# Performance work log

Hardware: AMD Instinct MI355X
Metric: run time of the kernel (lower is better)

Reference implementation:

```python
import jax, jax.numpy as jnp
import numpy as np

D = 1024
H = 16
HD = D // H
B = 2
T = 2048


def _rope_tables(t, hd):
    inv_freq = 1.0 / (10000.0 ** (np.arange(0, hd, 2, dtype=np.float32) / hd))
    ang = np.arange(t, dtype=np.float32)[:, None] * inv_freq[None, :]  # [T, hd/2]
    emb = np.concatenate([ang, ang], axis=-1)  # [T, hd]
    return jnp.asarray(np.cos(emb)), jnp.asarray(np.sin(emb))


def setup_inputs() -> dict:
    key = jax.random.key(0)
    kx, kq, kk, kv, ko = jax.random.split(key, 5)
    scale = 0.02
    x = jax.random.normal(kx, (B, T, D), dtype=jnp.float32)
    cos, sin = _rope_tables(T, HD)
    mask = jnp.tril(jnp.ones((T, T), dtype=jnp.int32))[None, None]  # [1,1,T,T]
    wq = jax.random.normal(kq, (D, D), dtype=jnp.float32) * scale
    wk = jax.random.normal(kk, (D, D), dtype=jnp.float32) * scale
    wv = jax.random.normal(kv, (D, D), dtype=jnp.float32) * scale
    wo = jax.random.normal(ko, (D, D), dtype=jnp.float32) * scale
    return {"x": x, "cos": cos, "sin": sin, "mask": mask,
            "wq": wq, "wk": wk, "wv": wv, "wo": wo}


def _rotate_half(t):
    t1, t2 = jnp.split(t, 2, axis=-1)
    return jnp.concatenate((-t2, t1), axis=-1)


def reference(x, cos, sin, mask, wq, wk, wv, wo):
    Bx, Tx, C = x.shape
    hd = C // H
    # nn.Linear: y = x @ W.T  -> [B,T,H,hd] -> [B,H,T,hd]
    q = (x @ wq.T).reshape(Bx, Tx, H, hd).transpose(0, 2, 1, 3)
    k = (x @ wk.T).reshape(Bx, Tx, H, hd).transpose(0, 2, 1, 3)
    v = (x @ wv.T).reshape(Bx, Tx, H, hd).transpose(0, 2, 1, 3)
    c = cos[:Tx][None, None]  # [1,1,T,hd]
    s = sin[:Tx][None, None]
    q = q * c + _rotate_half(q) * s
    k = k * c + _rotate_half(k) * s
    att = jnp.einsum('bhqd,bhkd->bhqk', q, k) * (hd ** -0.5)
    att = jnp.where(mask[:, :, :Tx, :Tx] == 0, -jnp.inf, att)
    att = jax.nn.softmax(att, axis=-1)
    out = jnp.einsum('bhqk,bhkd->bhqd', att, v)
    out = out.transpose(0, 2, 1, 3).reshape(Bx, Tx, C)
    return out @ wo.T
```

## Files before the change

kernel.cpp:

```cpp
#include <hip/hip_runtime.h>
#include <math.h>

constexpr int D  = 1024;
constexpr int H  = 16;
constexpr int HD = 64;
constexpr int B  = 2;
constexpr int T  = 2048;
constexpr int M  = B * T;

constexpr size_t XSZ = (size_t)M * D;
constexpr size_t WSZ = (size_t)D * D;

typedef float  f32x4   __attribute__((ext_vector_type(4)));
typedef float  f32x16  __attribute__((ext_vector_type(16)));
typedef __bf16 bf16x8  __attribute__((ext_vector_type(8)));
typedef __bf16 bf16x4  __attribute__((ext_vector_type(4)));
typedef unsigned u32x2 __attribute__((ext_vector_type(2)));
typedef unsigned u32x4 __attribute__((ext_vector_type(4)));

static __device__ inline f32x4 mfma16(bf16x8 a, bf16x8 b, f32x4 c) {
  return __builtin_amdgcn_mfma_f32_16x16x32_bf16(a, b, c, 0, 0, 0);
}
static __device__ inline f32x16 mfma32(bf16x8 a, bf16x8 b, f32x16 c) {
  return __builtin_amdgcn_mfma_f32_32x32x16_bf16(a, b, c, 0, 0, 0);
}
static __device__ inline unsigned cvtpk(float a, float b) {
  unsigned r;
  asm("v_cvt_pk_bf16_f32 %0, %1, %2" : "=v"(r) : "v"(a), "v"(b));
  return r;
}
static __device__ inline u32x2 plswap(unsigned a, unsigned b) {
  return __builtin_amdgcn_permlane32_swap(a, b, false, false);
}
static __device__ inline void gload16(const __bf16* g, __bf16* l) {
  __builtin_amdgcn_global_load_lds(
      (const __attribute__((address_space(1))) void*)g,
      (__attribute__((address_space(3))) void*)l, 16, 0, 0);
}

__global__ __launch_bounds__(256)
void cvt_all(const float* __restrict__ x, const float* __restrict__ wq,
             const float* __restrict__ wk, const float* __restrict__ wv,
             const float* __restrict__ wo, __bf16* __restrict__ out) {
  size_t idx = ((size_t)blockIdx.x * 256 + threadIdx.x) * 8;
  const float* src;
  if      (idx < XSZ)            src = x  + idx;
  else if (idx < XSZ + WSZ)      src = wq + (idx - XSZ);
  else if (idx < XSZ + 2 * WSZ)  src = wk + (idx - XSZ - WSZ);
  else if (idx < XSZ + 3 * WSZ)  src = wv + (idx - XSZ - 2 * WSZ);
  else                           src = wo + (idx - XSZ - 3 * WSZ);
  float4 a = *reinterpret_cast<const float4*>(src);
  float4 b = *reinterpret_cast<const float4*>(src + 4);
  bf16x8 o;
  o[0] = (__bf16)a.x; o[1] = (__bf16)a.y; o[2] = (__bf16)a.z; o[3] = (__bf16)a.w;
  o[4] = (__bf16)b.x; o[5] = (__bf16)b.y; o[6] = (__bf16)b.z; o[7] = (__bf16)b.w;
  *reinterpret_cast<bf16x8*>(out + idx) = o;
}

template<int MODE>
__global__ __launch_bounds__(256)
void gemm_mfma(const __bf16* __restrict__ A,
               const __bf16* __restrict__ W0, const __bf16* __restrict__ W1,
               const __bf16* __restrict__ W2,
               const float* __restrict__ cosT, const float* __restrict__ sinT,
               void* __restrict__ out0, void* __restrict__ out1,
               void* __restrict__ out2) {
  __shared__ __bf16 As[128 * 64];
  __shared__ __bf16 Bs[128 * 64];

  const int tid  = threadIdx.x;
  const int lane = tid & 63;
  const int w    = tid >> 6;
  const int wm   = w >> 1;
  const int wn   = w & 1;
  const int l15  = lane & 15, lg = lane >> 4;
  const int m0   = blockIdx.y * 128;

  int which, n0;
  const __bf16* Bw;
  if (MODE == 1) {
    which = blockIdx.x >> 3;
    n0 = (blockIdx.x & 7) * 128;
    Bw = which == 0 ? W0 : which == 1 ? W1 : W2;
  } else {
    which = 0;
    n0 = blockIdx.x * 128;
    Bw = W0;
  }

  f32x4 acc[4][4];
  #pragma unroll
  for (int i = 0; i < 4; ++i)
    #pragma unroll
    for (int j = 0; j < 4; ++j) acc[i][j] = (f32x4){0.f, 0.f, 0.f, 0.f};

  const int r0 = tid >> 3;
  const int c0 = (tid & 7) * 8;

  for (int k0 = 0; k0 < 1024; k0 += 64) {
    #pragma unroll
    for (int i = 0; i < 4; ++i) {
      gload16(A  + (size_t)(m0 + r0 + 32 * i) * 1024 + k0 + c0,
              As + (tid + 256 * i) * 8);
      gload16(Bw + (size_t)(n0 + r0 + 32 * i) * 1024 + k0 + c0,
              Bs + (tid + 256 * i) * 8);
    }
    __syncthreads();

    #pragma unroll
    for (int ks = 0; ks < 2; ++ks) {
      bf16x8 af[4], bfr[4];
      #pragma unroll
      for (int mt = 0; mt < 4; ++mt)
        af[mt] = *reinterpret_cast<const bf16x8*>(
            &As[(wm * 64 + mt * 16 + l15) * 64 + ks * 32 + lg * 8]);
      #pragma unroll
      for (int nt = 0; nt < 4; ++nt)
        bfr[nt] = *reinterpret_cast<const bf16x8*>(
            &Bs[(wn * 64 + nt * 16 + l15) * 64 + ks * 32 + lg * 8]);
      #pragma unroll
      for (int mt = 0; mt < 4; ++mt)
        #pragma unroll
        for (int nt = 0; nt < 4; ++nt)
          acc[mt][nt] = mfma16(af[mt], bfr[nt], acc[mt][nt]);
    }
    __syncthreads();
  }

  if (MODE == 0) {
    float* o = (float*)out0;
    #pragma unroll
    for (int mt = 0; mt < 4; ++mt) {
      const int mb = m0 + wm * 64 + mt * 16 + lg * 4;
      #pragma unroll
      for (int nt = 0; nt < 4; ++nt) {
        const int n = n0 + wn * 64 + nt * 16 + l15;
        #pragma unroll
        for (int r = 0; r < 4; ++r)
          o[(size_t)(mb + r) * 1024 + n] = acc[mt][nt][r];
      }
    }
  } else if (which < 2) {
    __bf16* dst = which == 0 ? (__bf16*)out0 : (__bf16*)out1;
    const float qs = (which == 0) ? 0.180336880f : 1.0f;
    const int h = (n0 + wn * 64) >> 6;
    #pragma unroll
    for (int mt = 0; mt < 4; ++mt) {
      const int tb   = m0 + wm * 64 + mt * 16 + lg * 4;
      const int bb   = tb >> 11;
      const int tloc = tb & 2047;
      #pragma unroll
      for (int r = 0; r < 4; ++r) {
        const int t = tloc + r;
        #pragma unroll
        for (int nt = 0; nt < 2; ++nt) {
          const int hd = nt * 16 + l15;
          const float c = cosT[t * HD + hd];
          const float s = sinT[t * HD + hd];
          const float v1 = acc[mt][nt][r];
          const float v2 = acc[mt][nt + 2][r];
          const size_t base = (((size_t)(bb * H + h)) * T + t) * HD;
          dst[base + hd]      = (__bf16)((v1 * c - v2 * s) * qs);
          dst[base + hd + 32] = (__bf16)((v2 * c + v1 * s) * qs);
        }
      }
    }
  } else {
    __bf16* dst = (__bf16*)out2;
    const int h = (n0 + wn * 64) >> 6;
    #pragma unroll
    for (int mt = 0; mt < 4; ++mt) {
      const int tb = m0 + wm * 64 + mt * 16 + lg * 4;
      const int bb = tb >> 11;
      const int t0 = tb & 2047;
      #pragma unroll
      for (int nt = 0; nt < 4; ++nt) {
        const int hd = nt * 16 + l15;
        bf16x4 ov;
        #pragma unroll
        for (int r = 0; r < 4; ++r) ov[r] = (__bf16)acc[mt][nt][r];
        *reinterpret_cast<bf16x4*>(
            &dst[(((size_t)(bb * H + h)) * HD + hd) * T + t0]) = ov;
      }
    }
  }
}

__global__ __launch_bounds__(256, 2)
void attn_v12(const __bf16* __restrict__ Q, const __bf16* __restrict__ K,
              const __bf16* __restrict__ Vt, __bf16* __restrict__ Ob) {
  const int tid  = threadIdx.x;
  const int lane = tid & 63;
  const int w    = tid >> 6;
  const int l31  = lane & 31;
  const int hi   = lane >> 5;
  const int bx   = blockIdx.x;
  const int by   = blockIdx.y;
  const int bh   = (bx & 7) + 8 * (by >> 3);
  const int x    = (bx >> 3) + 2 * (by & 7);

  const int wi = (bh < 16) ? w : (w ^ 1);
  const int qt = (wi == 0) ? 2 * x : (wi == 1) ? 63 - 2 * x
               : (wi == 2) ? 2 * x + 1 : 62 - 2 * x;
  const int q0w = qt * 32;
  const int NT  = (qt >> 1) + 1;

  const __bf16* Qg = Q  + (size_t)bh * T * HD;
  const __bf16* Kg = K  + (size_t)bh * T * HD;
  const __bf16* Vg = Vt + (size_t)bh * HD * T;

  bf16x8 qfr[4];
  #pragma unroll
  for (int st = 0; st < 4; ++st)
    qfr[st] = *reinterpret_cast<const bf16x8*>(
        Qg + (size_t)(q0w + l31) * HD + st * 16 + hi * 8);

  f32x16 zv;
  #pragma unroll
  for (int i = 0; i < 16; ++i) zv[i] = 0.f;

  float m_run = -INFINITY, l_run = 0.f;
  f32x16 oacc0, oacc1;
  #pragma unroll
  for (int i = 0; i < 16; ++i) { oacc0[i] = 0.f; oacc1[i] = 0.f; }

  const __bf16* kbase = Kg + (size_t)l31 * HD + hi * 8;
  const __bf16* vbase = Vg + (size_t)l31 * T + hi * 8;

#define LOADK8(K0, K1, K2, K3, K4, K5, K6, K7, jj)                            \
  do {                                                                        \
    const __bf16* _kp = kbase + (size_t)(jj) * 64 * HD;                       \
    K0 = *reinterpret_cast<const bf16x8*>(_kp);                               \
    K1 = *reinterpret_cast<const bf16x8*>(_kp + 16);                          \
    K2 = *reinterpret_cast<const bf16x8*>(_kp + 32);                          \
    K3 = *reinterpret_cast<const bf16x8*>(_kp + 48);                          \
    const __bf16* _kq = _kp + (size_t)32 * HD;                                \
    K4 = *reinterpret_cast<const bf16x8*>(_kq);                               \
    K5 = *reinterpret_cast<const bf16x8*>(_kq + 16);                          \
    K6 = *reinterpret_cast<const bf16x8*>(_kq + 32);                          \
    K7 = *reinterpret_cast<const bf16x8*>(_kq + 48);                          \
  } while (0)

#define TILE64(K0, K1, K2, K3, K4, K5, K6, K7, jj)                            \
  do {                                                                        \
             \
    const __bf16* _vp = vbase + (size_t)(jj) * 64;                            \
    bf16x8 Va00 = *reinterpret_cast<const bf16x8*>(_vp);                      \
    bf16x8 Va01 = *reinterpret_cast<const bf16x8*>(_vp + 16);                 \
    bf16x8 Va10 = *reinterpret_cast<const bf16x8*>(_vp + (size_t)32 * T);     \
    bf16x8 Va11 = *reinterpret_cast<const bf16x8*>(_vp + (size_t)32 * T + 16);\
    bf16x8 Vb00 = *reinterpret_cast<const bf16x8*>(_vp + 32);                 \
    bf16x8 Vb01 = *reinterpret_cast<const bf16x8*>(_vp + 48);                 \
    bf16x8 Vb10 = *reinterpret_cast<const bf16x8*>(_vp + (size_t)32 * T + 32);\
    bf16x8 Vb11 = *reinterpret_cast<const bf16x8*>(_vp + (size_t)32 * T + 48);\
               \
    f32x16 s0a = mfma32(K0, qfr[0], zv);                                      \
    f32x16 s0b = mfma32(K1, qfr[1], zv);                                      \
    f32x16 s1a = mfma32(K4, qfr[0], zv);                                      \
    f32x16 s1b = mfma32(K5, qfr[1], zv);                                      \
    s0a = mfma32(K2, qfr[2], s0a);                                            \
    s0b = mfma32(K3, qfr[3], s0b);                                            \
    s1a = mfma32(K6, qfr[2], s1a);                                            \
    s1b = mfma32(K7, qfr[3], s1b);                                            \
    f32x16 sv0, sv1;                                                          \
    _Pragma("unroll")                                                         \
    for (int _i = 0; _i < 16; ++_i) {                                         \
      sv0[_i] = s0a[_i] + s0b[_i];                                            \
      sv1[_i] = s1a[_i] + s1b[_i];                                            \
    }                                                                         \
    if ((jj) == NT - 1) {         \
      const int _q  = q0w + l31;                                              \
      const int _k0 = (jj) * 64 + 4 * hi;                                     \
      _Pragma("unroll")                                                       \
      for (int _r = 0; _r < 16; ++_r) {                                       \
        const int _key = _k0 + (_r & 3) + 8 * (_r >> 2);                      \
        if (_key > _q)      sv0[_r] = -INFINITY;                              \
        if (_key + 32 > _q) sv1[_r] = -INFINITY;                              \
      }                                                                       \
    }                                                                         \
                                             \
    float _mx[16];                                                            \
    _Pragma("unroll")                                                         \
    for (int _i = 0; _i < 16; ++_i) _mx[_i] = fmaxf(sv0[_i], sv1[_i]);        \
    _Pragma("unroll")                                                         \
    for (int _s = 8; _s > 0; _s >>= 1)                                        \
      _Pragma("unroll")                                                       \
      for (int _i = 0; _i < 8; ++_i)                                          \
        if (_i < _s) _mx[_i] = fmaxf(_mx[_i], _mx[_i + _s]);                  \
    union { float f; unsigned u; } _cv; _cv.f = _mx[0];                       \
    u32x2 _sw = plswap(_cv.u, _cv.u);                                         \
    union { unsigned u; float f; } _c0, _c1; _c0.u = _sw[0]; _c1.u = _sw[1];  \
    const float _pmax = fmaxf(_c0.f, _c1.f);                                  \
    if (__any(_pmax > m_run + 8.f)) {                                         \
      const float _mn = fmaxf(m_run, _pmax);                                  \
      const float _rs = exp2f(m_run - _mn);                                   \
      l_run *= _rs;                                                           \
      _Pragma("unroll")                                                       \
      for (int _i = 0; _i < 16; ++_i) { oacc0[_i] *= _rs; oacc1[_i] *= _rs; } \
      m_run = _mn;                                                            \
    }                                                                         \
    _Pragma("unroll")                                                         \
    for (int _i = 0; _i < 16; ++_i) {                                         \
      sv0[_i] = exp2f(sv0[_i] - m_run);                                       \
      sv1[_i] = exp2f(sv1[_i] - m_run);                                       \
    }                                                                         \
    float _sm[16];                                                            \
    _Pragma("unroll")                                                         \
    for (int _i = 0; _i < 16; ++_i) _sm[_i] = sv0[_i] + sv1[_i];              \
    _Pragma("unroll")                                                         \
    for (int _s = 8; _s > 0; _s >>= 1)                                        \
      _Pragma("unroll")                                                       \
      for (int _i = 0; _i < 8; ++_i)                                          \
        if (_i < _s) _sm[_i] += _sm[_i + _s];                                 \
    l_run += _sm[0];                                                          \
    unsigned _cp0[8], _cp1[8];                                                \
    _Pragma("unroll")                                                         \
    for (int _m = 0; _m < 4; ++_m) {                                          \
      _cp0[2 * _m]     = cvtpk(sv0[4 * _m],     sv0[4 * _m + 1]);             \
      _cp0[2 * _m + 1] = cvtpk(sv0[4 * _m + 2], sv0[4 * _m + 3]);             \
      _cp1[2 * _m]     = cvtpk(sv1[4 * _m],     sv1[4 * _m + 1]);             \
      _cp1[2 * _m + 1] = cvtpk(sv1[4 * _m + 2], sv1[4 * _m + 3]);             \
    }                                                                         \
    {                                                                         \
      u32x2 _r0 = plswap(_cp0[0], _cp0[2]);                                   \
      u32x2 _r1 = plswap(_cp0[1], _cp0[3]);                                   \
      union { u32x4 u; bf16x8 v; } _pu;                                       \
      _pu.u = (u32x4){_r0[0], _r1[0], _r0[1], _r1[1]};                        \
      oacc0 = mfma32(Va00, _pu.v, oacc0);                                     \
      oacc1 = mfma32(Va10, _pu.v, oacc1);                                     \
    }                                                                         \
    {                                                                         \
      u32x2 _r0 = plswap(_cp0[4], _cp0[6]);                                   \
      u32x2 _r1 = plswap(_cp0[5], _cp0[7]);                                   \
      union { u32x4 u; bf16x8 v; } _pu;                                       \
      _pu.u = (u32x4){_r0[0], _r1[0], _r0[1], _r1[1]};                        \
      oacc0 = mfma32(Va01, _pu.v, oacc0);                                     \
      oacc1 = mfma32(Va11, _pu.v, oacc1);                                     \
    }                                                                         \
    {                                                                         \
      u32x2 _r0 = plswap(_cp1[0], _cp1[2]);                                   \
      u32x2 _r1 = plswap(_cp1[1], _cp1[3]);                                   \
      union { u32x4 u; bf16x8 v; } _pu;                                       \
      _pu.u = (u32x4){_r0[0], _r1[0], _r0[1], _r1[1]};                        \
      oacc0 = mfma32(Vb00, _pu.v, oacc0);                                     \
      oacc1 = mfma32(Vb10, _pu.v, oacc1);                                     \
    }                                                                         \
    {                                                                         \
      u32x2 _r0 = plswap(_cp1[4], _cp1[6]);                                   \
      u32x2 _r1 = plswap(_cp1[5], _cp1[7]);                                   \
      union { u32x4 u; bf16x8 v; } _pu;                                       \
      _pu.u = (u32x4){_r0[0], _r1[0], _r0[1], _r1[1]};                        \
      oacc0 = mfma32(Vb01, _pu.v, oacc0);                                     \
      oacc1 = mfma32(Vb11, _pu.v, oacc1);                                     \
    }                                                                         \
  } while (0)

  bf16x8 kA0, kA1, kA2, kA3, kA4, kA5, kA6, kA7;
  bf16x8 kB0, kB1, kB2, kB3, kB4, kB5, kB6, kB7;

  LOADK8(kA0, kA1, kA2, kA3, kA4, kA5, kA6, kA7, 0);
  int j = 0;
  #pragma unroll 1
  for (;;) {
    if (j + 1 < NT) LOADK8(kB0, kB1, kB2, kB3, kB4, kB5, kB6, kB7, j + 1);
    TILE64(kA0, kA1, kA2, kA3, kA4, kA5, kA6, kA7, j);
    if (++j >= NT) break;
    if (j + 1 < NT) LOADK8(kA0, kA1, kA2, kA3, kA4, kA5, kA6, kA7, j + 1);
    TILE64(kB0, kB1, kB2, kB3, kB4, kB5, kB6, kB7, j);
    if (++j >= NT) break;
  }
#undef TILE64
#undef LOADK8

  const float l_tot = l_run + __shfl_xor(l_run, 32);
  const float inv = 1.f / l_tot;
  const int b = bh >> 4, h = bh & 15;
  const int q_abs = q0w + l31;
  const size_t rowbase = ((size_t)(b * T + q_abs)) * 1024 + h * 64;
  #pragma unroll
  for (int rg = 0; rg < 4; ++rg) {
    bf16x4 o0, o1;
    #pragma unroll
    for (int r = 0; r < 4; ++r) {
      o0[r] = (__bf16)(oacc0[rg * 4 + r] * inv);
      o1[r] = (__bf16)(oacc1[rg * 4 + r] * inv);
    }
    *reinterpret_cast<bf16x4*>(&Ob[rowbase + rg * 8 + hi * 4])      = o0;
    *reinterpret_cast<bf16x4*>(&Ob[rowbase + 32 + rg * 8 + hi * 4]) = o1;
  }
}

extern "C" void kernel_launch(void* const* d_in, const int* in_sizes, int n_in,
                              void* d_out, int out_size, void* d_ws, size_t ws_size,
                              hipStream_t stream) {
  const float* x    = (const float*)d_in[0];
  const float* cosT = (const float*)d_in[1];
  const float* sinT = (const float*)d_in[2];
  const float* wq   = (const float*)d_in[4];
  const float* wk   = (const float*)d_in[5];
  const float* wv   = (const float*)d_in[6];
  const float* wo   = (const float*)d_in[7];
  float* out = (float*)d_out;

  __bf16* xb   = (__bf16*)d_ws;
  __bf16* wqb  = xb  + XSZ;
  __bf16* wkb  = wqb + WSZ;
  __bf16* wvb  = wkb + WSZ;
  __bf16* wob  = wvb + WSZ;
  __bf16* Qh   = wob + WSZ;
  __bf16* Kh   = Qh  + XSZ;
  __bf16* Vth  = Kh  + XSZ;
  __bf16* attb = Vth + XSZ;

  cvt_all<<<(XSZ + 4 * WSZ) / 8 / 256, 256, 0, stream>>>(x, wq, wk, wv, wo, xb);

  gemm_mfma<1><<<dim3(24, 32), 256, 0, stream>>>(
      xb, wqb, wkb, wvb, cosT, sinT, Qh, Kh, Vth);

  attn_v12<<<dim3(16, 32), 256, 0, stream>>>(Qh, Kh, Vth, attb);

  gemm_mfma<0><<<dim3(8, 32), 256, 0, stream>>>(
      attb, wob, nullptr, nullptr, nullptr, nullptr, out, nullptr, nullptr);
}
```

Before: 156.3 us.

## Store Q/K/V in MFMA fragment-major layout for contiguous attention loads

The QKV projection epilogue now writes Q, K and V directly in a fragment-ordered layout of 512-element blocks, one per lane-fragment, instead of row-major [bh,T,HD] and transposed V. The attention kernel can then load each MFMA operand with a single fully contiguous 16-byte-per-lane access at fixed 512-element strides, instead of strided row gathers. The aim is better coalescing and simpler addressing in the attention inner loop. The cost is scattered, less coalesced stores in the GEMM epilogue, along with more complex index math there.

```diff
diff --git a/kernel.cpp b/kernel.cpp
--- a/kernel.cpp
+++ b/kernel.cpp
@@ -144,14 +144,23 @@
     __bf16* dst = which == 0 ? (__bf16*)out0 : (__bf16*)out1;
     const float qs = (which == 0) ? 0.180336880f : 1.0f;
     const int h = (n0 + wn * 64) >> 6;
+    const int e  = l15 & 7;
+    const int Lh = (l15 >> 3) << 5;
     #pragma unroll
     for (int mt = 0; mt < 4; ++mt) {
       const int tb   = m0 + wm * 64 + mt * 16 + lg * 4;
       const int bb   = tb >> 11;
       const int tloc = tb & 2047;
+      const int bh   = bb * H + h;
       #pragma unroll
       for (int r = 0; r < 4; ++r) {
         const int t = tloc + r;
+        const int L = (t & 31) + Lh;
+        size_t fb;
+        if (MODE == 1 && which == 0)
+          fb = ((size_t)bh * 64 + (t >> 5)) * 4;
+        else
+          fb = (((size_t)bh * 32 + (t >> 6)) * 2 + ((t >> 5) & 1)) * 4;
         #pragma unroll
         for (int nt = 0; nt < 2; ++nt) {
           const int hd = nt * 16 + l15;
@@ -159,9 +168,8 @@
           const float s = sinT[t * HD + hd];
           const float v1 = acc[mt][nt][r];
           const float v2 = acc[mt][nt + 2][r];
-          const size_t base = (((size_t)(bb * H + h)) * T + t) * HD;
-          dst[base + hd]      = (__bf16)((v1 * c - v2 * s) * qs);
-          dst[base + hd + 32] = (__bf16)((v2 * c + v1 * s) * qs);
+          dst[(fb + nt)     * 512 + L * 8 + e] = (__bf16)((v1 * c - v2 * s) * qs);
+          dst[(fb + nt + 2) * 512 + L * 8 + e] = (__bf16)((v2 * c + v1 * s) * qs);
         }
       }
     }
@@ -170,25 +178,33 @@
     const int h = (n0 + wn * 64) >> 6;
     #pragma unroll
     for (int mt = 0; mt < 4; ++mt) {
-      const int tb = m0 + wm * 64 + mt * 16 + lg * 4;
-      const int bb = tb >> 11;
-      const int t0 = tb & 2047;
+      const int tb   = m0 + wm * 64 + mt * 16 + lg * 4;
+      const int bb   = tb >> 11;
+      const int tloc = tb & 2047;
+      const int bh   = bb * H + h;
+      const int jt   = tloc >> 6;
+      const int kt   = tloc & 63;
+      const int Lk   = ((kt >> 3) & 1) << 5;
+      const int e0   = kt & 7;
+      const size_t fb = (((size_t)bh * 32 + jt) * 2) * 4 + (kt >> 4);
       #pragma unroll
       for (int nt = 0; nt < 4; ++nt) {
         const int hd = nt * 16 + l15;
+        const int dg = hd >> 5;
+        const int L  = (hd & 31) + Lk;
         bf16x4 ov;
         #pragma unroll
         for (int r = 0; r < 4; ++r) ov[r] = (__bf16)acc[mt][nt][r];
         *reinterpret_cast<bf16x4*>(
-            &dst[(((size_t)(bb * H + h)) * HD + hd) * T + t0]) = ov;
+            &dst[(fb + (size_t)dg * 4) * 512 + L * 8 + e0]) = ov;
       }
     }
   }
 }
 
 __global__ __launch_bounds__(256, 2)
-void attn_v12(const __bf16* __restrict__ Q, const __bf16* __restrict__ K,
-              const __bf16* __restrict__ Vt, __bf16* __restrict__ Ob) {
+void attn_v13(const __bf16* __restrict__ Qf, const __bf16* __restrict__ Kf,
+              const __bf16* __restrict__ Vf, __bf16* __restrict__ Ob) {
   const int tid  = threadIdx.x;
   const int lane = tid & 63;
   const int w    = tid >> 6;
@@ -205,15 +221,11 @@
   const int q0w = qt * 32;
   const int NT  = (qt >> 1) + 1;
 
-  const __bf16* Qg = Q  + (size_t)bh * T * HD;
-  const __bf16* Kg = K  + (size_t)bh * T * HD;
-  const __bf16* Vg = Vt + (size_t)bh * HD * T;
-
+  const __bf16* qbase = Qf + (((size_t)bh * 64 + qt) * 4) * 512 + lane * 8;
   bf16x8 qfr[4];
   #pragma unroll
   for (int st = 0; st < 4; ++st)
-    qfr[st] = *reinterpret_cast<const bf16x8*>(
-        Qg + (size_t)(q0w + l31) * HD + st * 16 + hi * 8);
+    qfr[st] = *reinterpret_cast<const bf16x8*>(qbase + st * 512);
 
   f32x16 zv;
   #pragma unroll
@@ -224,35 +236,34 @@
   #pragma unroll
   for (int i = 0; i < 16; ++i) { oacc0[i] = 0.f; oacc1[i] = 0.f; }
 
-  const __bf16* kbase = Kg + (size_t)l31 * HD + hi * 8;
-  const __bf16* vbase = Vg + (size_t)l31 * T + hi * 8;
+  const __bf16* kbase = Kf + ((size_t)bh * 32 * 8) * 512 + lane * 8;
+  const __bf16* vbase = Vf + ((size_t)bh * 32 * 8) * 512 + lane * 8;
 
 #define LOADK8(K0, K1, K2, K3, K4, K5, K6, K7, jj)                            \
   do {                                                                        \
-    const __bf16* _kp = kbase + (size_t)(jj) * 64 * HD;                       \
+    const __bf16* _kp = kbase + (size_t)(jj) * 8 * 512;                       \
     K0 = *reinterpret_cast<const bf16x8*>(_kp);                               \
-    K1 = *reinterpret_cast<const bf16x8*>(_kp + 16);                          \
-    K2 = *reinterpret_cast<const bf16x8*>(_kp + 32);                          \
-    K3 = *reinterpret_cast<const bf16x8*>(_kp + 48);                          \
-    const __bf16* _kq = _kp + (size_t)32 * HD;                                \
-    K4 = *reinterpret_cast<const bf16x8*>(_kq);                               \
-    K5 = *reinterpret_cast<const bf16x8*>(_kq + 16);                          \
-    K6 = *reinterpret_cast<const bf16x8*>(_kq + 32);                          \
-    K7 = *reinterpret_cast<const bf16x8*>(_kq + 48);                          \
+    K1 = *reinterpret_cast<const bf16x8*>(_kp + 512);                         \
+    K2 = *reinterpret_cast<const bf16x8*>(_kp + 1024);                        \
+    K3 = *reinterpret_cast<const bf16x8*>(_kp + 1536);                        \
+    K4 = *reinterpret_cast<const bf16x8*>(_kp + 2048);                        \
+    K5 = *reinterpret_cast<const bf16x8*>(_kp + 2560);                        \
+    K6 = *reinterpret_cast<const bf16x8*>(_kp + 3072);                        \
+    K7 = *reinterpret_cast<const bf16x8*>(_kp + 3584);                        \
   } while (0)
 
 #define TILE64(K0, K1, K2, K3, K4, K5, K6, K7, jj)                            \
   do {                                                                        \
              \
-    const __bf16* _vp = vbase + (size_t)(jj) * 64;                            \
+    const __bf16* _vp = vbase + (size_t)(jj) * 8 * 512;                       \
     bf16x8 Va00 = *reinterpret_cast<const bf16x8*>(_vp);                      \
-    bf16x8 Va01 = *reinterpret_cast<const bf16x8*>(_vp + 16);                 \
-    bf16x8 Va10 = *reinterpret_cast<const bf16x8*>(_vp + (size_t)32 * T);     \
-    bf16x8 Va11 = *reinterpret_cast<const bf16x8*>(_vp + (size_t)32 * T + 16);\
-    bf16x8 Vb00 = *reinterpret_cast<const bf16x8*>(_vp + 32);                 \
-    bf16x8 Vb01 = *reinterpret_cast<const bf16x8*>(_vp + 48);                 \
-    bf16x8 Vb10 = *reinterpret_cast<const bf16x8*>(_vp + (size_t)32 * T + 32);\
-    bf16x8 Vb11 = *reinterpret_cast<const bf16x8*>(_vp + (size_t)32 * T + 48);\
+    bf16x8 Va01 = *reinterpret_cast<const bf16x8*>(_vp + 512);                \
+    bf16x8 Vb00 = *reinterpret_cast<const bf16x8*>(_vp + 1024);               \
+    bf16x8 Vb01 = *reinterpret_cast<const bf16x8*>(_vp + 1536);               \
+    bf16x8 Va10 = *reinterpret_cast<const bf16x8*>(_vp + 2048);               \
+    bf16x8 Va11 = *reinterpret_cast<const bf16x8*>(_vp + 2560);               \
+    bf16x8 Vb10 = *reinterpret_cast<const bf16x8*>(_vp + 3072);               \
+    bf16x8 Vb11 = *reinterpret_cast<const bf16x8*>(_vp + 3584);               \
                \
     f32x16 s0a = mfma32(K0, qfr[0], zv);                                      \
     f32x16 s0b = mfma32(K1, qfr[1], zv);                                      \
@@ -407,17 +418,17 @@
   __bf16* wkb  = wqb + WSZ;
   __bf16* wvb  = wkb + WSZ;
   __bf16* wob  = wvb + WSZ;
-  __bf16* Qh   = wob + WSZ;
-  __bf16* Kh   = Qh  + XSZ;
-  __bf16* Vth  = Kh  + XSZ;
-  __bf16* attb = Vth + XSZ;
+  __bf16* Qfb  = wob + WSZ;
+  __bf16* Kfb  = Qfb + XSZ;
+  __bf16* Vfb  = Kfb + XSZ;
+  __bf16* attb = Vfb + XSZ;
 
   cvt_all<<<(XSZ + 4 * WSZ) / 8 / 256, 256, 0, stream>>>(x, wq, wk, wv, wo, xb);
 
   gemm_mfma<1><<<dim3(24, 32), 256, 0, stream>>>(
-      xb, wqb, wkb, wvb, cosT, sinT, Qh, Kh, Vth);
-
-  attn_v12<<<dim3(16, 32), 256, 0, stream>>>(Qh, Kh, Vth, attb);
+      xb, wqb, wkb, wvb, cosT, sinT, Qfb, Kfb, Vfb);
+
+  attn_v13<<<dim3(16, 32), 256, 0, stream>>>(Qfb, Kfb, Vfb, attb);
 
   gemm_mfma<0><<<dim3(8, 32), 256, 0, stream>>>(
       attb, wob, nullptr, nullptr, nullptr, nullptr, out, nullptr, nullptr);
```

Measured after the change: 146.0 us. -6.6%, faster.
